# Performance work log

Measured on AMD Instinct MI355X. Metric: run time of the kernel, lower is better.

Reference implementation:

```python
import jax, jax.numpy as jnp
import numpy as np
from jax import lax

B, K, D = 4, 9, 33
DN = ('NCHW', 'OIHW', 'NCHW')


def conv2d(x, w, b, pad, stride=1):
    y = lax.conv_general_dilated(x, w, (stride, stride), [(pad, pad), (pad, pad)],
                                 dimension_numbers=DN)
    return y + b[None, :, None, None]


def conv_t2d(x, w, b):
    # torch ConvTranspose2d(k=4, s=2, p=1); w layout [Cin, Cout, 4, 4]
    w2 = jnp.transpose(jnp.flip(w, (2, 3)), (1, 0, 2, 3))
    y = lax.conv_general_dilated(x, w2, (1, 1), [(2, 2), (2, 2)], lhs_dilation=(2, 2),
                                 dimension_numbers=DN)
    return y + b[None, :, None, None]


def tri_sample(luts, img01):
    # luts: [K,3,D,D,D]; img01: [B,3,H,W] in [0,1]
    # grid_sample semantics: channel R indexes last LUT axis, G middle, B first;
    # align_corners=True -> pos = c*(D-1); border padding -> clip indices.
    Dn = luts.shape[-1]
    pos = img01 * (Dn - 1)
    i0f = jnp.floor(pos)
    i0 = jnp.clip(i0f.astype(jnp.int32), 0, Dn - 1)
    i1 = jnp.clip(i0 + 1, 0, Dn - 1)
    f = pos - i0f
    r0, g0, b0 = i0[:, 0], i0[:, 1], i0[:, 2]
    r1, g1, b1 = i1[:, 0], i1[:, 1], i1[:, 2]
    fr, fg, fb = f[:, 0], f[:, 1], f[:, 2]

    def g(ib, ig, ir):
        return luts[:, :, ib, ig, ir]  # [K,3,B,H,W]

    def w(a):
        return a[None, None]

    return (g(b0, g0, r0) * w((1 - fb) * (1 - fg) * (1 - fr))
          + g(b0, g0, r1) * w((1 - fb) * (1 - fg) * fr)
          + g(b0, g1, r0) * w((1 - fb) * fg * (1 - fr))
          + g(b0, g1, r1) * w((1 - fb) * fg * fr)
          + g(b1, g0, r0) * w(fb * (1 - fg) * (1 - fr))
          + g(b1, g0, r1) * w(fb * (1 - fg) * fr)
          + g(b1, g1, r0) * w(fb * fg * (1 - fr))
          + g(b1, g1, r1) * w(fb * fg * fr))  # [K,3,B,H,W]


def tv3d(luts):
    # vectorized TV_3D over all K LUTs; per-lut means summed over K
    Dn = luts.shape[-1]
    wr = np.ones((3, Dn, Dn, Dn - 1), np.float32); wr[:, :, :, 0] *= 2; wr[:, :, :, -1] *= 2
    wg = np.ones((3, Dn, Dn - 1, Dn), np.float32); wg[:, :, 0, :] *= 2; wg[:, :, -1, :] *= 2
    wb = np.ones((3, Dn - 1, Dn, Dn), np.float32); wb[:, 0] *= 2; wb[:, -1] *= 2
    dr = luts[..., :-1] - luts[..., 1:]
    dg = luts[..., :-1, :] - luts[..., 1:, :]
    db = luts[:, :, :-1] - luts[:, :, 1:]
    ax = (1, 2, 3, 4)
    tv = (jnp.mean(dr ** 2 * wr[None], ax) + jnp.mean(dg ** 2 * wg[None], ax)
          + jnp.mean(db ** 2 * wb[None], ax)).sum()
    mn = (jnp.mean(jax.nn.relu(dr), ax) + jnp.mean(jax.nn.relu(dg), ax)
          + jnp.mean(jax.nn.relu(db), ax)).sum()
    return tv, mn


def setup_inputs() -> dict:
    key = jax.random.key(0)
    k1, k2 = jax.random.split(key)
    feat_map = jax.random.normal(k1, (B, 320, 64, 64), jnp.float32)
    img = jax.random.uniform(k2, (B, 3, 512, 512), jnp.float32, -1.0, 1.0)
    rng = np.random.default_rng(0)
    p = lambda *s: jnp.asarray(rng.normal(0, 0.05, s).astype(np.float32))
    bz = lambda n: jnp.asarray(rng.normal(0, 0.01, (n,)).astype(np.float32))
    # identity LUT for lut 0 (as in torch init), small random for the rest
    c = np.linspace(0, 1, D, dtype=np.float32)
    ident = np.stack(np.meshgrid(c, c, c, indexing='ij'), 0)  # [3,D,D,D]
    luts = np.concatenate([ident[None], rng.normal(0, 0.02, (K - 1, 3, D, D, D)).astype(np.float32)], 0)
    return {
        'feat_map': feat_map, 'img': img,
        'conv_out_w': p(4, 320, 3, 3), 'conv_out_b': bz(4),
        'r1_w': p(K, 320, 1, 1), 'r1_b': bz(K),
        'r2_w': p(K, K, 3, 3), 'r2_b': bz(K),
        'rt1_w': p(K, K, 4, 4), 'rt1_b': bz(K),
        'r3_w': p(K, K, 3, 3), 'r3_b': bz(K),
        'rt2_w': p(K, K, 4, 4), 'rt2_b': bz(K),
        'r4_w': p(K, K, 3, 3), 'r4_b': bz(K),
        'rt3_w': p(K, K, 4, 4), 'rt3_b': bz(K),
        'luts': jnp.asarray(luts),
        'f1_w': p(64, 3, 3, 3), 'f1_b': bz(64),
        'f2_w': p(3, 64, 3, 3), 'f2_b': bz(3),
    }


def reference(feat_map, img, conv_out_w, conv_out_b, r1_w, r1_b, r2_w, r2_b,
              rt1_w, rt1_b, r3_w, r3_b, rt2_w, rt2_b, r4_w, r4_b, rt3_w, rt3_b,
              luts, f1_w, f1_b, f2_w, f2_b):
    noise_pred = conv2d(feat_map, conv_out_w, conv_out_b, 1)  # [B,4,64,64]
    r = jax.nn.relu(conv2d(feat_map, r1_w, r1_b, 0))
    r = jax.nn.relu(conv2d(r, r2_w, r2_b, 1))
    r = conv_t2d(r, rt1_w, rt1_b)                     # 64 -> 128
    r = jax.nn.relu(conv2d(r, r3_w, r3_b, 1))
    r = conv_t2d(r, rt2_w, rt2_b)                     # 128 -> 256
    r = jax.nn.relu(conv2d(r, r4_w, r4_b, 1))
    r = conv_t2d(r, rt3_w, rt3_b)                     # 256 -> 512
    R = jax.nn.softmax(r, axis=1)                     # [B,K,512,512]
    dh = R[..., :-1] - R[..., 1:]
    dw = R[..., :-1, :] - R[..., 1:, :]
    tv_R = jnp.abs(dh).mean() + jnp.abs(dw).mean()
    img01 = img * 0.5 + 0.5
    lut_stack = tri_sample(luts, img01)               # [K,3,B,H,W]
    lut_image = jnp.einsum('kcbhw,bkhw->bchw', lut_stack, R)
    h = jax.nn.relu(conv2d(lut_image, f1_w, f1_b, 1))
    lut_image = conv2d(h, f2_w, f2_b, 1)              # [B,3,512,512]
    weights_norm = jnp.mean(R ** 2)
    tv_c, mn_c = tv3d(luts)
    reg_loss = 0.001 * (weights_norm + tv_c + tv_R) + 10.0 * mn_c
    return noise_pred, lut_image, reg_loss
```

## Files before the change

### kernel.cpp

```cpp
#include <hip/hip_runtime.h>
#include <hip/hip_fp16.h>
#include <hip/hip_fp8.h>

#define NPIX 262144

#if defined(__has_builtin)
#if __has_builtin(__builtin_amdgcn_cvt_f32_fp8)
#define HAVE_FP8_CVT 1
#endif
#endif

__device__ inline float fp8_byte_to_f(unsigned int w, int sel) {
#ifdef HAVE_FP8_CVT
  switch (sel & 3) {
    case 0: return __builtin_amdgcn_cvt_f32_fp8(w, 0);
    case 1: return __builtin_amdgcn_cvt_f32_fp8(w, 1);
    case 2: return __builtin_amdgcn_cvt_f32_fp8(w, 2);
    default: return __builtin_amdgcn_cvt_f32_fp8(w, 3);
  }
#else
  __hip_fp8_e4m3 q;
  q.__x = (unsigned char)((w >> (8 * sel)) & 0xff);
  return (float)q;
#endif
}

__device__ inline __half2 relu2(__half2 a) {
  __half2 r;
  unsigned int z = 0;
  asm volatile("v_pk_max_f16 %0, %1, %2" : "=v"(r) : "v"(a), "v"(z));
  return r;
}

__device__ inline float block_sum(float v, float* sm) {
  #pragma unroll
  for (int off = 32; off > 0; off >>= 1) v += __shfl_down(v, off, 64);
  int lane = threadIdx.x & 63, wid = threadIdx.x >> 6;
  __syncthreads();
  if (lane == 0) sm[wid] = v;
  __syncthreads();
  float r = 0.f;
  if (threadIdx.x < 4) r = sm[threadIdx.x];
  r += __shfl_down(r, 2, 64);
  r += __shfl_down(r, 1, 64);
  return r;
}

__global__ __launch_bounds__(256) void k_init_noise(const float* __restrict__ bias,
                                                    float* __restrict__ out) {
  int i = blockIdx.x * 256 + threadIdx.x;
  int c = (i >> 12) & 3;
  out[i] = bias[c];
}

__global__ __launch_bounds__(256) void k_conv_noise(const float* __restrict__ feat,
                                                    const float* __restrict__ w,
                                                    float* __restrict__ out) {
  __shared__ float tile[16][324];
  __shared__ float wl[576];
  int b = blockIdx.y, c0 = blockIdx.z * 16;
  int tx = threadIdx.x & 15, ty = threadIdx.x >> 4;
  int tx0 = (blockIdx.x & 3) << 4, ty0 = (blockIdx.x >> 2) << 4;
  for (int i = threadIdx.x; i < 16 * 324; i += 256) {
    int ci = i / 324, rem = i % 324;
    int r = rem / 18, cc = rem % 18;
    int gy = ty0 + r - 1, gx = tx0 + cc - 1;
    float v = 0.f;
    if (gy >= 0 && gy < 64 && gx >= 0 && gx < 64)
      v = feat[((b * 320 + c0 + ci) * 64 + gy) * 64 + gx];
    tile[ci][rem] = v;
  }
  for (int i = threadIdx.x; i < 576; i += 256) {
    int o = i / 144, rem = i % 144;
    int cl = rem / 9, t = rem % 9;
    wl[i] = w[o * 2880 + (c0 + cl) * 9 + t];
  }
  __syncthreads();
  float acc[4] = {0.f, 0.f, 0.f, 0.f};
  for (int ci = 0; ci < 16; ++ci) {
    #pragma unroll
    for (int kh = 0; kh < 3; ++kh)
      #pragma unroll
      for (int kw = 0; kw < 3; ++kw) {
        float v = tile[ci][(ty + kh) * 18 + tx + kw];
        #pragma unroll
        for (int o = 0; o < 4; ++o)
          acc[o] = fmaf(v, wl[o * 144 + ci * 9 + kh * 3 + kw], acc[o]);
      }
  }
  int y = ty0 + ty, x = tx0 + tx;
  #pragma unroll
  for (int o = 0; o < 4; ++o)
    atomicAdd(&out[((b * 4 + o) * 64 + y) * 64 + x], acc[o]);
}

__global__ __launch_bounds__(256) void k_r1(const float* __restrict__ feat,
                                            const float* __restrict__ w,
                                            float* __restrict__ out) {
  __shared__ float wl[576];
  int c0 = blockIdx.y * 64;
  for (int i = threadIdx.x; i < 576; i += 256) {
    int k = i / 64, cl = i % 64;
    wl[i] = w[k * 320 + c0 + cl];
  }
  __syncthreads();
  int pix = blockIdx.x * 256 + threadIdx.x;
  int b = pix >> 12, hw = pix & 4095;
  float acc[9] = {};
  const float* fp = feat + ((size_t)(b * 320 + c0)) * 4096 + hw;
  for (int c = 0; c < 64; ++c) {
    float v = fp[c * 4096];
    #pragma unroll
    for (int k = 0; k < 9; ++k) acc[k] = fmaf(v, wl[k * 64 + c], acc[k]);
  }
  float* op = out + (size_t)(b * 9) * 4096 + hw;
  #pragma unroll
  for (int k = 0; k < 9; ++k) atomicAdd(&op[k * 4096], acc[k]);
}

__global__ __launch_bounds__(256) void k_conv9(const float* __restrict__ in,
                                               const float* __restrict__ w9,
                                               const float* __restrict__ bias,
                                               float* __restrict__ out, int H,
                                               const float* __restrict__ prebias) {
  __shared__ float tile[9][324];
  __shared__ float wl[729];
  __shared__ float bl[9];
  __shared__ float pbl[9];
  int b = blockIdx.y;
  int tilesx = H >> 4;
  int tx0 = (blockIdx.x % tilesx) << 4, ty0 = (blockIdx.x / tilesx) << 4;
  int tx = threadIdx.x & 15, ty = threadIdx.x >> 4;
  for (int i = threadIdx.x; i < 729; i += 256) wl[i] = w9[i];
  if (threadIdx.x < 9) {
    bl[threadIdx.x] = bias[threadIdx.x];
    pbl[threadIdx.x] = prebias ? prebias[threadIdx.x] : 0.f;
  }
  __syncthreads();
  for (int i = threadIdx.x; i < 9 * 324; i += 256) {
    int ci = i / 324, rem = i % 324;
    int r = rem / 18, cc = rem % 18;
    int gy = ty0 + r - 1, gx = tx0 + cc - 1;
    float v = 0.f;
    if (gy >= 0 && gy < H && gx >= 0 && gx < H) {
      v = in[((size_t)(b * 9 + ci) * H + gy) * H + gx];
      if (prebias) v = fmaxf(v + pbl[ci], 0.f);
    }
    tile[ci][rem] = v;
  }
  __syncthreads();
  float acc[9] = {};
  for (int ci = 0; ci < 9; ++ci) {
    #pragma unroll
    for (int kh = 0; kh < 3; ++kh)
      #pragma unroll
      for (int kw = 0; kw < 3; ++kw) {
        float v = tile[ci][(ty + kh) * 18 + tx + kw];
        #pragma unroll
        for (int k = 0; k < 9; ++k)
          acc[k] = fmaf(v, wl[(k * 9 + ci) * 9 + kh * 3 + kw], acc[k]);
      }
  }
  int y = ty0 + ty, x = tx0 + tx;
  #pragma unroll
  for (int k = 0; k < 9; ++k)
    out[((size_t)(b * 9 + k) * H + y) * H + x] = fmaxf(acc[k] + bl[k], 0.f);
}

__global__ __launch_bounds__(256) void k_convt9(const float* __restrict__ in,
                                                const float* __restrict__ wt,
                                                const float* __restrict__ bias,
                                                float* __restrict__ out, int Hin) {
  __shared__ float tile[9][100];
  __shared__ float wl[1296];
  __shared__ float bl[9];
  int b = blockIdx.y;
  int Hout = Hin * 2;
  int tilesx = Hout >> 4;
  int tx0 = (blockIdx.x % tilesx) << 4, ty0 = (blockIdx.x / tilesx) << 4;
  int tx = threadIdx.x & 15, ty = threadIdx.x >> 4;
  int ihb = (ty0 >> 1) - 1, iwb = (tx0 >> 1) - 1;
  for (int i = threadIdx.x; i < 1296; i += 256) wl[i] = wt[i];
  if (threadIdx.x < 9) bl[threadIdx.x] = bias[threadIdx.x];
  for (int i = threadIdx.x; i < 900; i += 256) {
    int ci = i / 100, rem = i % 100;
    int r = rem / 10, cc = rem % 10;
    int gy = ihb + r, gx = iwb + cc;
    float v = 0.f;
    if (gy >= 0 && gy < Hin && gx >= 0 && gx < Hin)
      v = in[((size_t)(b * 9 + ci) * Hin + gy) * Hin + gx];
    tile[ci][rem] = v;
  }
  __syncthreads();
  int oy = ty0 + ty, ox = tx0 + tx;
  int p = oy & 1, q = ox & 1;
  int lr0 = ((oy + p - 2) >> 1) - ihb;
  int lc0 = ((ox + q - 2) >> 1) - iwb;
  float acc[9] = {};
  for (int ci = 0; ci < 9; ++ci) {
    #pragma unroll
    for (int a = 0; a < 2; ++a) {
      int kh = p + 2 * a, lr = lr0 + a;
      #pragma unroll
      for (int e = 0; e < 2; ++e) {
        int kw = q + 2 * e, lc = lc0 + e;
        float v = tile[ci][lr * 10 + lc];
        #pragma unroll
        for (int k = 0; k < 9; ++k)
          acc[k] = fmaf(v, wl[((ci * 9 + k) * 4 + (3 - kh)) * 4 + (3 - kw)], acc[k]);
      }
    }
  }
  #pragma unroll
  for (int k = 0; k < 9; ++k)
    out[((size_t)(b * 9 + k) * Hout + oy) * Hout + ox] = acc[k] + bl[k];
}

__global__ __launch_bounds__(256) void k_lut_pack(const float* __restrict__ luts,
                                                  unsigned char* __restrict__ lutpk) {
  int cell = blockIdx.x * 256 + threadIdx.x;
  if (cell >= 35937) return;
  unsigned char out[32];
  #pragma unroll
  for (int c = 0; c < 3; ++c) {
    unsigned short u = __half_as_ushort(__float2half(luts[c * 35937 + cell]));
    out[2 * c] = (unsigned char)(u & 0xff);
    out[2 * c + 1] = (unsigned char)(u >> 8);
  }
  #pragma unroll
  for (int e = 3; e < 27; ++e) {
    __hip_fp8_e4m3 q(luts[e * 35937 + cell]);
    out[6 + (e - 3)] = q.__x;
  }
  out[30] = 0;
  out[31] = 0;
  uint4* dst = (uint4*)(lutpk + (size_t)cell * 32);
  dst[0] = *(const uint4*)(out);
  dst[1] = *(const uint4*)(out + 16);
}

__global__ __launch_bounds__(256) void k_w_pack(const float* __restrict__ w1,
                                                const float* __restrict__ w2,
                                                __half2* __restrict__ w1r,
                                                __half2* __restrict__ w2r) {
  int t = blockIdx.x * 256 + threadIdx.x;
  if (t < 864) {
    int ii = t >> 5, j = t & 31;
    w1r[t] = __floats2half2_rn(w1[(2 * j) * 27 + ii], w1[(2 * j + 1) * 27 + ii]);
  } else if (t < 1728) {
    int i = t - 864;
    int tap = i / 96, rem = i % 96;
    int o = rem >> 5, j = rem & 31;
    w2r[i] = __floats2half2_rn(w2[o * 576 + (2 * j) * 9 + tap],
                               w2[o * 576 + (2 * j + 1) * 9 + tap]);
  }
}

__global__ __launch_bounds__(256) void k_softmax_tri(const float* __restrict__ in,
                                                     const float* __restrict__ img,
                                                     const unsigned char* __restrict__ lutpk,
                                                     __half* __restrict__ R,
                                                     __half* __restrict__ lutp,
                                                     float* __restrict__ p_sq) {
  __shared__ float sm[4];
  int tg = blockIdx.x * 256 + threadIdx.x;
  int b = tg >> 18, hw = tg & (NPIX - 1);
  const float* ip = in + (size_t)(b * 9) * NPIX + hw;
  float v[9];
  float m = -1e30f;
  #pragma unroll
  for (int k = 0; k < 9; ++k) { v[k] = ip[(size_t)k * NPIX]; m = fmaxf(m, v[k]); }
  float s = 0.f;
  #pragma unroll
  for (int k = 0; k < 9; ++k) { v[k] = expf(v[k] - m); s += v[k]; }
  float inv = 1.f / s;
  float sq = 0.f;
  __half* rp = R + (size_t)(b * 9) * NPIX + hw;
  #pragma unroll
  for (int k = 0; k < 9; ++k) {
    v[k] *= inv;
    rp[(size_t)k * NPIX] = __float2half(v[k]);
    sq += v[k] * v[k];
  }
  int i0[3], i1[3];
  float f[3];
  #pragma unroll
  for (int c = 0; c < 3; ++c) {
    float x = img[(size_t)(b * 3 + c) * NPIX + hw];
    float pos = (x * 0.5f + 0.5f) * 32.f;
    float fl = floorf(pos);
    int ii = (int)fl;
    ii = min(max(ii, 0), 32);
    i0[c] = ii;
    i1[c] = min(ii + 1, 32);
    f[c] = pos - fl;
  }
  float fr = f[0], fg = f[1], fb = f[2];
  int cells[8];
  float wt8[8];
  cells[0] = (i0[2] * 33 + i0[1]) * 33 + i0[0]; wt8[0] = (1 - fb) * (1 - fg) * (1 - fr);
  cells[1] = (i0[2] * 33 + i0[1]) * 33 + i1[0]; wt8[1] = (1 - fb) * (1 - fg) * fr;
  cells[2] = (i0[2] * 33 + i1[1]) * 33 + i0[0]; wt8[2] = (1 - fb) * fg * (1 - fr);
  cells[3] = (i0[2] * 33 + i1[1]) * 33 + i1[0]; wt8[3] = (1 - fb) * fg * fr;
  cells[4] = (i1[2] * 33 + i0[1]) * 33 + i0[0]; wt8[4] = fb * (1 - fg) * (1 - fr);
  cells[5] = (i1[2] * 33 + i0[1]) * 33 + i1[0]; wt8[5] = fb * (1 - fg) * fr;
  cells[6] = (i1[2] * 33 + i1[1]) * 33 + i0[0]; wt8[6] = fb * fg * (1 - fr);
  cells[7] = (i1[2] * 33 + i1[1]) * 33 + i1[0]; wt8[7] = fb * fg * fr;
  float acc[3] = {0.f, 0.f, 0.f};
  #pragma unroll
  for (int j = 0; j < 8; ++j) {
    const uint4* p = (const uint4*)(lutpk + (size_t)cells[j] * 32);
    uint4 q0 = p[0], q1 = p[1];
    float wv[9];
    #pragma unroll
    for (int k = 0; k < 9; ++k) wv[k] = wt8[j] * v[k];
    acc[0] = fmaf(wv[0], __half2float(__ushort_as_half((unsigned short)(q0.x & 0xffff))), acc[0]);
    acc[1] = fmaf(wv[0], __half2float(__ushort_as_half((unsigned short)(q0.x >> 16))), acc[1]);
    acc[2] = fmaf(wv[0], __half2float(__ushort_as_half((unsigned short)(q0.y & 0xffff))), acc[2]);
    unsigned int wrds[8] = {q0.x, q0.y, q0.z, q0.w, q1.x, q1.y, q1.z, q1.w};
    #pragma unroll
    for (int e = 3; e < 27; ++e) {
      const int byte = 6 + (e - 3);
      float fv = fp8_byte_to_f(wrds[byte >> 2], byte & 3);
      acc[e % 3] = fmaf(wv[e / 3], fv, acc[e % 3]);
    }
  }
  #pragma unroll
  for (int c = 0; c < 3; ++c)
    lutp[(size_t)(b * 3 + c) * NPIX + hw] = __float2half(acc[c]);
  float t = block_sum(sq, sm);
  if (threadIdx.x == 0) p_sq[blockIdx.x] = t;
}

__global__ __launch_bounds__(256) void k_tvr(const __half* __restrict__ R,
                                             float* __restrict__ p_tvr) {
  __shared__ float sm[4];
  int tg = blockIdx.x * 256 + threadIdx.x;
  float s = 0.f;
  for (int it = 0; it < 36; ++it) {
    size_t e = (size_t)it * 262144 + tg;
    int w = e & 511, h = (e >> 9) & 511;
    float v = __half2float(R[e]);
    if (w < 511) s += fabsf(v - __half2float(R[e + 1]));
    if (h < 511) s += fabsf(v - __half2float(R[e + 512]));
  }
  float t = block_sum(s, sm);
  if (threadIdx.x == 0) p_tvr[blockIdx.x] = t;
}

__global__ __launch_bounds__(256) void k_f1f2(const __half* __restrict__ lutp,
                                              const __half2* __restrict__ w1r,
                                              const float* __restrict__ b1,
                                              const __half2* __restrict__ w2r,
                                              const float* __restrict__ b2,
                                              float* __restrict__ outp) {
  __shared__ __half lutp_t[3][20][20];
  __shared__ __half hlds[324][72];
  int b = blockIdx.y;
  int tx0 = (blockIdx.x & 31) << 4, ty0 = (blockIdx.x >> 5) << 4;
  int t = threadIdx.x;
  for (int i = t; i < 1200; i += 256) {
    int ci = i / 400, rem = i % 400;
    int r = rem / 20, c = rem % 20;
    int gy = ty0 + r - 2, gx = tx0 + c - 2;
    __half v = __ushort_as_half((unsigned short)0);
    if (gy >= 0 && gy < 512 && gx >= 0 && gx < 512)
      v = lutp[(size_t)(b * 3 + ci) * NPIX + gy * 512 + gx];
    lutp_t[ci][r][c] = v;
  }
  __syncthreads();
  const __half2 z2 = __float2half2_rn(0.f);
  for (int hp = t; hp < 324; hp += 256) {
    int hy = hp / 18, hx = hp % 18;
    int gy = ty0 - 1 + hy, gx = tx0 - 1 + hx;
    __half2 acc[32];
    if (gy >= 0 && gy < 512 && gx >= 0 && gx < 512) {
      #pragma unroll
      for (int j = 0; j < 32; ++j)
        acc[j] = __floats2half2_rn(b1[2 * j], b1[2 * j + 1]);
      #pragma unroll
      for (int ci = 0; ci < 3; ++ci)
        #pragma unroll
        for (int kh = 0; kh < 3; ++kh)
          #pragma unroll
          for (int kw = 0; kw < 3; ++kw) {
            __half2 vv = __half2half2(lutp_t[ci][hy + kh][hx + kw]);
            const int ii = ci * 9 + kh * 3 + kw;
            #pragma unroll
            for (int j = 0; j < 32; ++j)
              acc[j] = __hfma2(vv, w1r[ii * 32 + j], acc[j]);
          }
      #pragma unroll
      for (int j = 0; j < 32; ++j) acc[j] = relu2(acc[j]);
    } else {
      #pragma unroll
      for (int j = 0; j < 32; ++j) acc[j] = z2;
    }
    __half2* dst = (__half2*)&hlds[hp][0];
    #pragma unroll
    for (int j = 0; j < 32; ++j) dst[j] = acc[j];
  }
  __syncthreads();
  int tyl = t >> 4, txl = t & 15;
  __half2 a0 = z2, a1 = z2, a2 = z2;
  #pragma unroll
  for (int kh = 0; kh < 3; ++kh)
    #pragma unroll
    for (int kw = 0; kw < 3; ++kw) {
      const int tap = kh * 3 + kw;
      int hp = (tyl + kh) * 18 + (txl + kw);
      const __half2* hrow = (const __half2*)&hlds[hp][0];
      #pragma unroll
      for (int j = 0; j < 32; ++j) {
        __half2 h2 = hrow[j];
        a0 = __hfma2(h2, w2r[tap * 96 + j], a0);
        a1 = __hfma2(h2, w2r[tap * 96 + 32 + j], a1);
        a2 = __hfma2(h2, w2r[tap * 96 + 64 + j], a2);
      }
    }
  int y = ty0 + tyl, x = tx0 + txl;
  outp[(size_t)(b * 3 + 0) * NPIX + y * 512 + x] = __low2float(a0) + __high2float(a0) + b2[0];
  outp[(size_t)(b * 3 + 1) * NPIX + y * 512 + x] = __low2float(a1) + __high2float(a1) + b2[1];
  outp[(size_t)(b * 3 + 2) * NPIX + y * 512 + x] = __low2float(a2) + __high2float(a2) + b2[2];
}

__global__ __launch_bounds__(256) void k_tv3d(const float* __restrict__ luts,
                                              float* __restrict__ p_tv,
                                              float* __restrict__ p_mn) {
  __shared__ float sm[4];
  float tv = 0.f, mn = 0.f;
  for (int it = 0; it < 8; ++it) {
    int e = it * 131072 + blockIdx.x * 256 + threadIdx.x;
    if (e < 970299) {
      int rem = e % 35937;
      int ib = rem / 1089, ig = (rem / 33) % 33, ir = rem % 33;
      float v = luts[e];
      if (ir < 32) {
        float d = v - luts[e + 1];
        float wgt = (ir == 0 || ir == 31) ? 2.f : 1.f;
        tv += wgt * d * d;
        mn += fmaxf(d, 0.f);
      }
      if (ig < 32) {
        float d = v - luts[e + 33];
        float wgt = (ig == 0 || ig == 31) ? 2.f : 1.f;
        tv += wgt * d * d;
        mn += fmaxf(d, 0.f);
      }
      if (ib < 32) {
        float d = v - luts[e + 1089];
        float wgt = (ib == 0 || ib == 31) ? 2.f : 1.f;
        tv += wgt * d * d;
        mn += fmaxf(d, 0.f);
      }
    }
  }
  float t1 = block_sum(tv, sm);
  float t2 = block_sum(mn, sm);
  if (threadIdx.x == 0) { p_tv[blockIdx.x] = t1; p_mn[blockIdx.x] = t2; }
}

__global__ __launch_bounds__(256) void k_final(const float* __restrict__ parts,
                                               float* __restrict__ out) {
  __shared__ float sm[4];
  float s_sq = 0.f, s_tvr = 0.f, s_tv = 0.f, s_mn = 0.f;
  for (int i = threadIdx.x; i < 4096; i += 256) s_sq += parts[i];
  for (int i = threadIdx.x; i < 1024; i += 256) s_tvr += parts[4096 + i];
  for (int i = threadIdx.x; i < 512; i += 256) s_tv += parts[5120 + i];
  for (int i = threadIdx.x; i < 512; i += 256) s_mn += parts[5632 + i];
  float t_sq = block_sum(s_sq, sm);
  float t_tvr = block_sum(s_tvr, sm);
  float t_tv = block_sum(s_tv, sm);
  float t_mn = block_sum(s_mn, sm);
  if (threadIdx.x == 0)
    out[0] = 0.001f * (t_sq / 9437184.f + t_tv / 104544.f + t_tvr / 9418752.f) +
             10.f * (t_mn / 104544.f);
}

extern "C" void kernel_launch(void* const* d_in, const int* in_sizes, int n_in,
                              void* d_out, int out_size, void* d_ws, size_t ws_size,
                              hipStream_t stream) {
  const float* feat = (const float*)d_in[0];
  const float* img = (const float*)d_in[1];
  const float* conv_out_w = (const float*)d_in[2];
  const float* conv_out_b = (const float*)d_in[3];
  const float* r1_w = (const float*)d_in[4];
  const float* r1_b = (const float*)d_in[5];
  const float* r2_w = (const float*)d_in[6];
  const float* r2_b = (const float*)d_in[7];
  const float* rt1_w = (const float*)d_in[8];
  const float* rt1_b = (const float*)d_in[9];
  const float* r3_w = (const float*)d_in[10];
  const float* r3_b = (const float*)d_in[11];
  const float* rt2_w = (const float*)d_in[12];
  const float* rt2_b = (const float*)d_in[13];
  const float* r4_w = (const float*)d_in[14];
  const float* r4_b = (const float*)d_in[15];
  const float* rt3_w = (const float*)d_in[16];
  const float* rt3_b = (const float*)d_in[17];
  const float* luts = (const float*)d_in[18];
  const float* f1_w = (const float*)d_in[19];
  const float* f1_b = (const float*)d_in[20];
  const float* f2_w = (const float*)d_in[21];
  const float* f2_b = (const float*)d_in[22];

  float* out_noise = (float*)d_out;
  float* out_img = out_noise + 65536;
  float* out_loss = out_img + 3145728;

  char* ws = (char*)d_ws;
  float* parts = (float*)ws;
  unsigned char* lutpk = (unsigned char*)(ws + 81920);
  __half2* w1r = (__half2*)(ws + 1232000);
  __half2* w2r = (__half2*)(ws + 1235456);
  float* bufA = (float*)(ws + 2381888);
  float* bufB = (float*)(ws + 40130624);
  __half* lutp = (__half*)(ws + 77879360);
  __half* Rh = (__half*)bufB;

  (void)hipMemsetAsync(bufA, 0, 589824 * 4, stream);

  k_lut_pack<<<141, 256, 0, stream>>>(luts, lutpk);
  k_w_pack<<<7, 256, 0, stream>>>(f1_w, f2_w, w1r, w2r);
  k_init_noise<<<256, 256, 0, stream>>>(conv_out_b, out_noise);
  k_conv_noise<<<dim3(16, 4, 20), 256, 0, stream>>>(feat, conv_out_w, out_noise);
  k_r1<<<dim3(64, 5), 256, 0, stream>>>(feat, r1_w, bufA);
  k_conv9<<<dim3(16, 4), 256, 0, stream>>>(bufA, r2_w, r2_b, bufB, 64, r1_b);
  k_convt9<<<dim3(64, 4), 256, 0, stream>>>(bufB, rt1_w, rt1_b, bufA, 64);
  k_conv9<<<dim3(64, 4), 256, 0, stream>>>(bufA, r3_w, r3_b, bufB, 128, nullptr);
  k_convt9<<<dim3(256, 4), 256, 0, stream>>>(bufB, rt2_w, rt2_b, bufA, 128);
  k_conv9<<<dim3(256, 4), 256, 0, stream>>>(bufA, r4_w, r4_b, bufB, 256, nullptr);
  k_convt9<<<dim3(1024, 4), 256, 0, stream>>>(bufB, rt3_w, rt3_b, bufA, 256);
  k_softmax_tri<<<4096, 256, 0, stream>>>(bufA, img, lutpk, Rh, lutp, parts);
  k_tvr<<<1024, 256, 0, stream>>>(Rh, parts + 4096);
  k_f1f2<<<dim3(1024, 4), 256, 0, stream>>>(lutp, w1r, f1_b, w2r, f2_b, out_img);
  k_tv3d<<<512, 256, 0, stream>>>(luts, parts + 5120, parts + 5632);
  k_final<<<1, 256, 0, stream>>>(parts, out_loss);
}
```

Measured before the change: 453.6 us.

## Move f1/f2 refinement convolutions onto MFMA 16x16x32 f16 instructions

Rewrites the fused f1→relu→f2 conv kernel so both convolutions run as implicit GEMMs on MFMA f16 instructions with fp32 accumulation, in place of per-thread packed half2 FMAs. Weights are prepacked into MFMA B-fragment layout, with padded K and N lanes zero-filled. The hidden tile is produced by 21 M-tiles per block, and the output conv does 18 MFMAs per pixel tile. The aim is to remove the large scalar FMA cost of the 64-channel hidden layer. In exchange it wastes compute on padding (27→32 inputs, 3→16 output columns) and changes the accumulation precision.

```diff
diff --git a/kernel.cpp b/kernel.cpp
--- a/kernel.cpp
+++ b/kernel.cpp
@@ -25,12 +25,9 @@
 #endif
 }
 
-__device__ inline __half2 relu2(__half2 a) {
-  __half2 r;
-  unsigned int z = 0;
-  asm volatile("v_pk_max_f16 %0, %1, %2" : "=v"(r) : "v"(a), "v"(z));
-  return r;
-}
+typedef __attribute__((ext_vector_type(8))) __fp16 half8;
+typedef __attribute__((ext_vector_type(4))) float f32x4;
+union FragCvt { uint4 u; half8 h; };
 
 __device__ inline float block_sum(float v, float* sm) {
   #pragma unroll
@@ -241,18 +238,37 @@
 
 __global__ __launch_bounds__(256) void k_w_pack(const float* __restrict__ w1,
                                                 const float* __restrict__ w2,
-                                                __half2* __restrict__ w1r,
-                                                __half2* __restrict__ w2r) {
+                                                uint4* __restrict__ w1frag,
+                                                uint4* __restrict__ w2frag) {
   int t = blockIdx.x * 256 + threadIdx.x;
-  if (t < 864) {
-    int ii = t >> 5, j = t & 31;
-    w1r[t] = __floats2half2_rn(w1[(2 * j) * 27 + ii], w1[(2 * j + 1) * 27 + ii]);
-  } else if (t < 1728) {
-    int i = t - 864;
-    int tap = i / 96, rem = i % 96;
-    int o = rem >> 5, j = rem & 31;
-    w2r[i] = __floats2half2_rn(w2[o * 576 + (2 * j) * 9 + tap],
-                               w2[o * 576 + (2 * j + 1) * 9 + tap]);
+  if (t < 256) {
+    int l = t & 63, nt = t >> 6;
+    int o = nt * 16 + (l & 15);
+    int kb = (l >> 4) * 8;
+    unsigned int u[4];
+    #pragma unroll
+    for (int j = 0; j < 4; ++j) {
+      int k0 = kb + 2 * j, k1 = k0 + 1;
+      unsigned short h0 = (k0 < 27) ? __half_as_ushort(__float2half(w1[o * 27 + k0])) : 0;
+      unsigned short h1 = (k1 < 27) ? __half_as_ushort(__float2half(w1[o * 27 + k1])) : 0;
+      u[j] = (unsigned)h0 | ((unsigned)h1 << 16);
+    }
+    w1frag[t] = make_uint4(u[0], u[1], u[2], u[3]);
+  } else if (t < 1408) {
+    int i2 = t - 256;
+    int s = i2 >> 6, l = i2 & 63;
+    int o = l & 15;
+    int tap = s >> 1;
+    int chb = (s & 1) * 32 + (l >> 4) * 8;
+    unsigned int u[4];
+    #pragma unroll
+    for (int j = 0; j < 4; ++j) {
+      int c0 = chb + 2 * j, c1 = c0 + 1;
+      unsigned short h0 = (o < 3) ? __half_as_ushort(__float2half(w2[o * 576 + c0 * 9 + tap])) : 0;
+      unsigned short h1 = (o < 3) ? __half_as_ushort(__float2half(w2[o * 576 + c1 * 9 + tap])) : 0;
+      u[j] = (unsigned)h0 | ((unsigned)h1 << 16);
+    }
+    w2frag[i2] = make_uint4(u[0], u[1], u[2], u[3]);
   }
 }
 
@@ -349,16 +365,16 @@
 }
 
 __global__ __launch_bounds__(256) void k_f1f2(const __half* __restrict__ lutp,
-                                              const __half2* __restrict__ w1r,
+                                              const uint4* __restrict__ w1frag,
                                               const float* __restrict__ b1,
-                                              const __half2* __restrict__ w2r,
+                                              const uint4* __restrict__ w2frag,
                                               const float* __restrict__ b2,
                                               float* __restrict__ outp) {
-  __shared__ __half lutp_t[3][20][20];
-  __shared__ __half hlds[324][72];
+  __shared__ __align__(16) _Float16 lutp_t[1208];
+  __shared__ __align__(16) _Float16 hlds[324 * 72];
   int b = blockIdx.y;
   int tx0 = (blockIdx.x & 31) << 4, ty0 = (blockIdx.x >> 5) << 4;
-  int t = threadIdx.x;
+  int t = threadIdx.x, lane = t & 63, wid = t >> 6;
   for (int i = t; i < 1200; i += 256) {
     int ci = i / 400, rem = i % 400;
     int r = rem / 20, c = rem % 20;
@@ -366,62 +382,81 @@
     __half v = __ushort_as_half((unsigned short)0);
     if (gy >= 0 && gy < 512 && gx >= 0 && gx < 512)
       v = lutp[(size_t)(b * 3 + ci) * NPIX + gy * 512 + gx];
-    lutp_t[ci][r][c] = v;
-  }
-  __syncthreads();
-  const __half2 z2 = __float2half2_rn(0.f);
-  for (int hp = t; hp < 324; hp += 256) {
-    int hy = hp / 18, hx = hp % 18;
-    int gy = ty0 - 1 + hy, gx = tx0 - 1 + hx;
-    __half2 acc[32];
-    if (gy >= 0 && gy < 512 && gx >= 0 && gx < 512) {
+    lutp_t[i] = *(const __fp16*)&v;
+  }
+  if (t < 8) lutp_t[1200 + t] = (_Float16)0.f;
+  int kb = (lane >> 4) * 8;
+  int off8[8];
+  #pragma unroll
+  for (int i = 0; i < 8; ++i) {
+    int k = kb + i;
+    off8[i] = (k < 27) ? ((k / 9) * 400 + ((k % 9) / 3) * 20 + (k % 3)) : -1;
+  }
+  FragCvt w1f[4];
+  #pragma unroll
+  for (int nt = 0; nt < 4; ++nt) w1f[nt].u = w1frag[nt * 64 + lane];
+  float bias1v[4];
+  #pragma unroll
+  for (int nt = 0; nt < 4; ++nt) bias1v[nt] = b1[nt * 16 + (lane & 15)];
+  bool interior = (tx0 > 0) && (tx0 < 496) && (ty0 > 0) && (ty0 < 496);
+  __syncthreads();
+  for (int mt = wid; mt < 21; mt += 4) {
+    int pr = mt * 16 + (lane & 15);
+    int pc = min(pr, 323);
+    int hy = pc / 18, hx = pc - hy * 18;
+    int base = hy * 20 + hx;
+    half8 af;
+    #pragma unroll
+    for (int i = 0; i < 8; ++i) {
+      int o_ = off8[i];
+      int addr = (o_ < 0) ? 1200 : (base + o_);
+      af[i] = lutp_t[addr];
+    }
+    #pragma unroll
+    for (int nt = 0; nt < 4; ++nt) {
+      f32x4 c = {bias1v[nt], bias1v[nt], bias1v[nt], bias1v[nt]};
+      c = __builtin_amdgcn_mfma_f32_16x16x32_f16(af, w1f[nt].h, c, 0, 0, 0);
       #pragma unroll
-      for (int j = 0; j < 32; ++j)
-        acc[j] = __floats2half2_rn(b1[2 * j], b1[2 * j + 1]);
+      for (int r = 0; r < 4; ++r) {
+        int px = mt * 16 + (lane >> 4) * 4 + r;
+        if (px < 324) {
+          float v = fmaxf(c[r], 0.f);
+          if (!interior) {
+            int hy2 = px / 18, hx2 = px - hy2 * 18;
+            int gy = ty0 - 1 + hy2, gx = tx0 - 1 + hx2;
+            if (gy < 0 || gy >= 512 || gx < 0 || gx >= 512) v = 0.f;
+          }
+          hlds[px * 72 + nt * 16 + (lane & 15)] = (_Float16)v;
+        }
+      }
+    }
+  }
+  FragCvt w2f[18];
+  #pragma unroll
+  for (int s = 0; s < 18; ++s) w2f[s].u = w2frag[s * 64 + lane];
+  int oc = lane & 15;
+  float bias2v = (oc < 3) ? b2[oc] : 0.f;
+  __syncthreads();
+  for (int mt = wid; mt < 16; mt += 4) {
+    int p = mt * 16 + (lane & 15);
+    int oy = p >> 4, ox = p & 15;
+    f32x4 acc = {bias2v, bias2v, bias2v, bias2v};
+    #pragma unroll
+    for (int s = 0; s < 18; ++s) {
+      int tap = s >> 1;
+      int hp = (oy + tap / 3) * 18 + ox + tap % 3;
+      const half8* ap = (const half8*)(hlds + hp * 72 + (s & 1) * 32 + kb);
+      acc = __builtin_amdgcn_mfma_f32_16x16x32_f16(*ap, w2f[s].h, acc, 0, 0, 0);
+    }
+    if (oc < 3) {
       #pragma unroll
-      for (int ci = 0; ci < 3; ++ci)
-        #pragma unroll
-        for (int kh = 0; kh < 3; ++kh)
-          #pragma unroll
-          for (int kw = 0; kw < 3; ++kw) {
-            __half2 vv = __half2half2(lutp_t[ci][hy + kh][hx + kw]);
-            const int ii = ci * 9 + kh * 3 + kw;
-            #pragma unroll
-            for (int j = 0; j < 32; ++j)
-              acc[j] = __hfma2(vv, w1r[ii * 32 + j], acc[j]);
-          }
-      #pragma unroll
-      for (int j = 0; j < 32; ++j) acc[j] = relu2(acc[j]);
-    } else {
-      #pragma unroll
-      for (int j = 0; j < 32; ++j) acc[j] = z2;
-    }
-    __half2* dst = (__half2*)&hlds[hp][0];
-    #pragma unroll
-    for (int j = 0; j < 32; ++j) dst[j] = acc[j];
-  }
-  __syncthreads();
-  int tyl = t >> 4, txl = t & 15;
-  __half2 a0 = z2, a1 = z2, a2 = z2;
-  #pragma unroll
-  for (int kh = 0; kh < 3; ++kh)
-    #pragma unroll
-    for (int kw = 0; kw < 3; ++kw) {
-      const int tap = kh * 3 + kw;
-      int hp = (tyl + kh) * 18 + (txl + kw);
-      const __half2* hrow = (const __half2*)&hlds[hp][0];
-      #pragma unroll
-      for (int j = 0; j < 32; ++j) {
-        __half2 h2 = hrow[j];
-        a0 = __hfma2(h2, w2r[tap * 96 + j], a0);
-        a1 = __hfma2(h2, w2r[tap * 96 + 32 + j], a1);
-        a2 = __hfma2(h2, w2r[tap * 96 + 64 + j], a2);
-      }
-    }
-  int y = ty0 + tyl, x = tx0 + txl;
-  outp[(size_t)(b * 3 + 0) * NPIX + y * 512 + x] = __low2float(a0) + __high2float(a0) + b2[0];
-  outp[(size_t)(b * 3 + 1) * NPIX + y * 512 + x] = __low2float(a1) + __high2float(a1) + b2[1];
-  outp[(size_t)(b * 3 + 2) * NPIX + y * 512 + x] = __low2float(a2) + __high2float(a2) + b2[2];
+      for (int r = 0; r < 4; ++r) {
+        int px = mt * 16 + (lane >> 4) * 4 + r;
+        int y = ty0 + (px >> 4), x = tx0 + (px & 15);
+        outp[(size_t)(b * 3 + oc) * NPIX + y * 512 + x] = acc[r];
+      }
+    }
+  }
 }
 
 __global__ __launch_bounds__(256) void k_tv3d(const float* __restrict__ luts,
@@ -511,8 +546,8 @@
   char* ws = (char*)d_ws;
   float* parts = (float*)ws;
   unsigned char* lutpk = (unsigned char*)(ws + 81920);
-  __half2* w1r = (__half2*)(ws + 1232000);
-  __half2* w2r = (__half2*)(ws + 1235456);
+  uint4* w1frag = (uint4*)(ws + 1232000);
+  uint4* w2frag = (uint4*)(ws + 1236096);
   float* bufA = (float*)(ws + 2381888);
   float* bufB = (float*)(ws + 40130624);
   __half* lutp = (__half*)(ws + 77879360);
@@ -521,7 +556,7 @@
   (void)hipMemsetAsync(bufA, 0, 589824 * 4, stream);
 
   k_lut_pack<<<141, 256, 0, stream>>>(luts, lutpk);
-  k_w_pack<<<7, 256, 0, stream>>>(f1_w, f2_w, w1r, w2r);
+  k_w_pack<<<6, 256, 0, stream>>>(f1_w, f2_w, w1frag, w2frag);
   k_init_noise<<<256, 256, 0, stream>>>(conv_out_b, out_noise);
   k_conv_noise<<<dim3(16, 4, 20), 256, 0, stream>>>(feat, conv_out_w, out_noise);
   k_r1<<<dim3(64, 5), 256, 0, stream>>>(feat, r1_w, bufA);
@@ -533,7 +568,7 @@
   k_convt9<<<dim3(1024, 4), 256, 0, stream>>>(bufB, rt3_w, rt3_b, bufA, 256);
   k_softmax_tri<<<4096, 256, 0, stream>>>(bufA, img, lutpk, Rh, lutp, parts);
   k_tvr<<<1024, 256, 0, stream>>>(Rh, parts + 4096);
-  k_f1f2<<<dim3(1024, 4), 256, 0, stream>>>(lutp, w1r, f1_b, w2r, f2_b, out_img);
+  k_f1f2<<<dim3(1024, 4), 256, 0, stream>>>(lutp, w1frag, f1_b, w2frag, f2_b, out_img);
   k_tv3d<<<512, 256, 0, stream>>>(luts, parts + 5120, parts + 5632);
   k_final<<<1, 256, 0, stream>>>(parts, out_loss);
 }
```

New measurement: 408.9 us. 9.8% less time.
